# Kernel tuning notes

Hardware: AMD Instinct MI355X
Metric: run time of the kernel (lower is better)

The kernel has to match this reference:

```python
import jax, jax.numpy as jnp
import numpy as np

D_MODEL, D_STATE, HEAD_DIM, EXPAND, K, N_GROUPS = 1024, 128, 64, 2, 4, 1
D_INNER = EXPAND * D_MODEL            # 2048
N_HEADS = D_INNER // HEAD_DIM         # 32
D_PROJ = 2 * D_INNER + 2 * N_GROUPS * D_STATE + N_HEADS  # 4384
EPS = 1e-6


def setup_inputs() -> dict:
    key = jax.random.key(0)
    ks = jax.random.split(key, 8)
    B, L = 2, 2048
    x = jax.random.normal(ks[0], (B, L, D_MODEL), dtype=jnp.float32)
    norm_w = jnp.ones((D_MODEL,), jnp.float32)
    in_proj_w = jax.random.normal(ks[1], (D_PROJ, D_MODEL), jnp.float32) * (D_MODEL ** -0.5)
    conv_w = jax.random.normal(ks[2], (D_INNER, 1, K), jnp.float32) * (K ** -0.5)
    conv_b = jnp.zeros((D_INNER,), jnp.float32)
    A_log = jnp.log(jax.random.uniform(ks[3], (N_HEADS,)) * 15.0 + 1.0)
    D = jnp.ones((N_HEADS,), jnp.float32)
    dt_bias = jnp.log(jax.random.uniform(ks[4], (N_HEADS,)) * 0.099 + 0.001)
    out_proj_w = jax.random.normal(ks[5], (D_MODEL, D_INNER), jnp.float32) * (D_INNER ** -0.5)
    return {"x": x, "norm_w": norm_w, "in_proj_w": in_proj_w, "conv_w": conv_w,
            "conv_b": conv_b, "A_log": A_log, "D": D, "dt_bias": dt_bias,
            "out_proj_w": out_proj_w}


def _silu(v):
    return v * jax.nn.sigmoid(v)


def reference(x, norm_w, in_proj_w, conv_w, conv_b, A_log, D, dt_bias, out_proj_w):
    Bsz, L, _ = x.shape
    residual = x
    # RMSNorm (pre-norm)
    xn = x * jax.lax.rsqrt(jnp.mean(x * x, axis=-1, keepdims=True) + EPS) * norm_w
    proj = xn @ in_proj_w.T                                     # (B, L, D_PROJ)
    # split fused projection -> (z, x_ssm, B, C, dt_raw)
    i = 0
    z = proj[..., i:i + D_INNER]; i += D_INNER
    x_ssm = proj[..., i:i + D_INNER]; i += D_INNER
    bc = N_GROUPS * D_STATE
    Bm = proj[..., i:i + bc].reshape(Bsz, L, N_GROUPS, D_STATE); i += bc
    Cm = proj[..., i:i + bc].reshape(Bsz, L, N_GROUPS, D_STATE); i += bc
    dt_raw = proj[..., i:i + N_HEADS]
    # causal depthwise conv1d (torch pad=K-1 then slice [:L] == left-pad K-1)
    xc = jnp.transpose(x_ssm, (0, 2, 1))                        # (B, D_INNER, L)
    xc = jax.lax.conv_general_dilated(
        xc, conv_w, window_strides=(1,), padding=[(K - 1, 0)],
        dimension_numbers=("NCH", "OIH", "NCH"), feature_group_count=D_INNER)
    xc = xc + conv_b[None, :, None]
    x_conv = _silu(jnp.transpose(xc, (0, 2, 1)))                # (B, L, D_INNER)
    # discretisation
    dt = jax.nn.softplus(dt_raw + dt_bias)                      # (B, L, H)
    dA = jnp.exp(-jnp.exp(A_log)[None, None, :] * dt)           # (B, L, H)
    x_heads = x_conv.reshape(Bsz, L, N_HEADS, HEAD_DIM)
    dt_x = dt[..., None] * x_heads                              # (B, L, H, P)
    group_idx = jnp.arange(N_HEADS) // (N_HEADS // N_GROUPS)
    Bg = Bm[:, :, group_idx, :]                                 # (B, L, H, N)
    Cg = Cm[:, :, group_idx, :]
    # sequential selective scan over time via lax.scan (fp32 state)
    def step(h, inp):
        dA_t, dtx_t, B_t, C_t = inp                             # (B,H),(B,H,P),(B,H,N),(B,H,N)
        h = h * dA_t[..., None, None] + dtx_t[..., None] * B_t[:, :, None, :]
        y_t = jnp.einsum("bhpn,bhn->bhp", h, C_t)
        return h, y_t
    h0 = jnp.zeros((Bsz, N_HEADS, HEAD_DIM, D_STATE), jnp.float32)
    xs = (jnp.moveaxis(dA, 1, 0).astype(jnp.float32),
          jnp.moveaxis(dt_x, 1, 0).astype(jnp.float32),
          jnp.moveaxis(Bg, 1, 0).astype(jnp.float32),
          jnp.moveaxis(Cg, 1, 0).astype(jnp.float32))
    _, y = jax.lax.scan(step, h0, xs)                           # y: (L, B, H, P)
    y = jnp.moveaxis(y, 0, 1).astype(x.dtype)                   # (B, L, H, P)
    y = y + D[None, None, :, None] * x_heads
    y = y.reshape(Bsz, L, D_INNER) * _silu(z)                   # gated output
    return residual + y @ out_proj_w.T
```

## Files before the change

kernel.cpp:

```cpp
#include <hip/hip_runtime.h>
#include <math.h>

#define B_SZ     2
#define L_SEQ    2048
#define DM       1024
#define DP       4384
#define PS       4480
#define DI       2048
#define NH       32
#define HD       64
#define DS       128
#define M_ROWS   (B_SZ * L_SEQ)
#define QCH      64
#define NC       (L_SEQ / QCH)

typedef __bf16 bf16x8 __attribute__((ext_vector_type(8)));
typedef __bf16 bf16x4 __attribute__((ext_vector_type(4)));
typedef __bf16 bf16x2 __attribute__((ext_vector_type(2)));
typedef float  f32x4  __attribute__((ext_vector_type(4)));

__device__ __forceinline__ void gload16(const void* g, void* l) {
    __builtin_amdgcn_global_load_lds(
        (const __attribute__((address_space(1))) unsigned int*)g,
        (__attribute__((address_space(3))) unsigned int*)l,
        16, 0, 0);
}

__global__ __launch_bounds__(256) void k_prep(const float* __restrict__ Wp,
                                              __bf16* __restrict__ Wpb,
                                              const float* __restrict__ x,
                                              const float* __restrict__ w,
                                              __bf16* __restrict__ xn) {
    int tid = threadIdx.x;
    if (blockIdx.x < 4384) {
        int i = blockIdx.x * 256 + tid;
        float4 v = ((const float4*)Wp)[i];
        bf16x4 o = { (__bf16)v.x, (__bf16)v.y, (__bf16)v.z, (__bf16)v.w };
        ((bf16x4*)Wpb)[i] = o;
        return;
    }
    int row = blockIdx.x - 4384;
    const float4* x4 = (const float4*)(x + (long)row * DM);
    float4 v = x4[tid];
    float ss = v.x * v.x + v.y * v.y + v.z * v.z + v.w * v.w;
    #pragma unroll
    for (int off = 32; off > 0; off >>= 1) ss += __shfl_xor(ss, off, 64);
    __shared__ float sred[4];
    if ((tid & 63) == 0) sred[tid >> 6] = ss;
    __syncthreads();
    float tot = sred[0] + sred[1] + sred[2] + sred[3];
    float scale = rsqrtf(tot * (1.0f / (float)DM) + 1e-6f);
    const float4* w4 = (const float4*)w;
    float4 wv = w4[tid];
    bf16x4 o = { (__bf16)(v.x * scale * wv.x), (__bf16)(v.y * scale * wv.y),
                 (__bf16)(v.z * scale * wv.z), (__bf16)(v.w * scale * wv.w) };
    ((bf16x4*)(xn + (long)row * DM))[tid] = o;
}

__global__ __launch_bounds__(256) void k_gemm_bf(const __bf16* __restrict__ A,
                                                 const __bf16* __restrict__ W,
                                                 __bf16* __restrict__ Cb,
                                                 float* __restrict__ Dt,
                                                 int Nw, int K, int ldc) {
    __shared__ __align__(16) __bf16 As[2][128 * 64];
    __shared__ __align__(16) __bf16 Bs[2][128 * 64];
    int t = threadIdx.x;

    int gx = gridDim.x;
    int nwg = gx * gridDim.y;
    int orig = blockIdx.y * gx + blockIdx.x;
    int wgid = (nwg & 7) ? orig : ((orig & 7) * (nwg >> 3) + (orig >> 3));
    int bx = wgid % gx, by = wgid / gx;
    int bm = by * 128, bn = bx * 128;

    int lane = t & 63, w = t >> 6;

    int rl = lane >> 3;
    int lc = (lane & 7) ^ rl;
    int rbase = w * 32 + rl;
    const __bf16* Agp[4];
    const __bf16* Wgp[4];
    #pragma unroll
    for (int i = 0; i < 4; i++) {
        Agp[i] = A + (long)(bm + rbase + i * 8) * K + lc * 8;
        int rb = bn + rbase + i * 8; if (rb >= Nw) rb = Nw - 1;
        Wgp[i] = W + (long)rb * K + lc * 8;
    }

    int wm = (w & 1) * 64, wn = (w >> 1) * 64;
    int ln = lane & 15;
    int q  = lane >> 4;

    f32x4 acc[4][4] = {};

    int nst = K >> 6;

    #pragma unroll
    for (int i = 0; i < 4; i++) {
        gload16(Agp[i], As[0] + (w * 4 + i) * 512);
        gload16(Wgp[i], Bs[0] + (w * 4 + i) * 512);
    }

    int cur = 0;
    for (int s = 0; s < nst; ++s) {
        if (s + 1 < nst) {
            long k1 = (long)(s + 1) << 6;
            #pragma unroll
            for (int i = 0; i < 4; i++) {
                gload16(Agp[i] + k1, As[cur ^ 1] + (w * 4 + i) * 512);
                gload16(Wgp[i] + k1, Bs[cur ^ 1] + (w * 4 + i) * 512);
            }
            asm volatile("s_waitcnt vmcnt(8)" ::: "memory");
        } else {
            asm volatile("s_waitcnt vmcnt(0)" ::: "memory");
        }
        __builtin_amdgcn_sched_barrier(0);
        __builtin_amdgcn_s_barrier();
        __builtin_amdgcn_sched_barrier(0);
        __builtin_amdgcn_s_setprio(1);

        const __bf16* Asc = As[cur];
        const __bf16* Bsc = Bs[cur];
        #pragma unroll
        for (int h = 0; h < 2; h++) {
            int ch = (4 * h + q);
            int koff = ((ch ^ (ln & 7)) << 3);
            bf16x8 af[4], bfr[4];
            #pragma unroll
            for (int i = 0; i < 4; i++)
                af[i]  = *(const bf16x8*)(Asc + (wm + ln + i * 16) * 64 + koff);
            #pragma unroll
            for (int j = 0; j < 4; j++)
                bfr[j] = *(const bf16x8*)(Bsc + (wn + ln + j * 16) * 64 + koff);
            #pragma unroll
            for (int i = 0; i < 4; i++)
                #pragma unroll
                for (int j = 0; j < 4; j++)
                    acc[i][j] = __builtin_amdgcn_mfma_f32_16x16x32_bf16(
                                    af[i], bfr[j], acc[i][j], 0, 0, 0);
        }
        __builtin_amdgcn_s_setprio(0);
        __builtin_amdgcn_sched_barrier(0);
        __builtin_amdgcn_s_barrier();
        __builtin_amdgcn_sched_barrier(0);
        cur ^= 1;
    }

    int colbase = bn + wn + ln;
    #pragma unroll
    for (int i = 0; i < 4; i++) {
        #pragma unroll
        for (int r = 0; r < 4; r++) {
            int m = bm + wm + i * 16 + (lane >> 4) * 4 + r;
            long off = (long)m * ldc + colbase;
            #pragma unroll
            for (int j = 0; j < 4; j++) {
                float v = acc[i][j][r];
                Cb[off + j * 16] = (__bf16)v;
                int col = colbase + j * 16;
                if (col >= 4352 && col < 4384)
                    Dt[(long)m * 32 + (col - 4352)] = v;
            }
        }
    }
}

__global__ __launch_bounds__(256) void k_gemm_out(const __bf16* __restrict__ A,
                                                  const __bf16* __restrict__ W,
                                                  const float* __restrict__ resid,
                                                  float* __restrict__ Cf,
                                                  int K, int ldc) {
    __shared__ __align__(16) __bf16 As[2][64 * 64];
    __shared__ __align__(16) __bf16 Bs[2][128 * 64];
    int t = threadIdx.x;

    int gx = gridDim.x;
    int nwg = gx * gridDim.y;
    int orig = blockIdx.y * gx + blockIdx.x;
    int wgid = (nwg & 7) ? orig : ((orig & 7) * (nwg >> 3) + (orig >> 3));
    int bx = wgid % gx, by = wgid / gx;
    int bm = by * 64, bn = bx * 128;

    int lane = t & 63, w = t >> 6;

    int rl = lane >> 3;
    int lc = (lane & 7) ^ rl;
    const __bf16* Agp[2];
    const __bf16* Wgp[4];
    #pragma unroll
    for (int i = 0; i < 2; i++)
        Agp[i] = A + (long)(bm + w * 16 + i * 8 + rl) * K + lc * 8;
    #pragma unroll
    for (int i = 0; i < 4; i++)
        Wgp[i] = W + (long)(bn + w * 32 + i * 8 + rl) * K + lc * 8;

    int wm = (w & 1) * 32, wn = (w >> 1) * 64;
    int ln = lane & 15;
    int q  = lane >> 4;

    f32x4 acc[2][4] = {};

    int nst = K >> 6;

    #pragma unroll
    for (int i = 0; i < 2; i++) gload16(Agp[i], As[0] + (w * 2 + i) * 512);
    #pragma unroll
    for (int i = 0; i < 4; i++) gload16(Wgp[i], Bs[0] + (w * 4 + i) * 512);

    int cur = 0;
    for (int s = 0; s < nst; ++s) {
        if (s + 1 < nst) {
            long k1 = (long)(s + 1) << 6;
            #pragma unroll
            for (int i = 0; i < 2; i++)
                gload16(Agp[i] + k1, As[cur ^ 1] + (w * 2 + i) * 512);
            #pragma unroll
            for (int i = 0; i < 4; i++)
                gload16(Wgp[i] + k1, Bs[cur ^ 1] + (w * 4 + i) * 512);
            asm volatile("s_waitcnt vmcnt(6)" ::: "memory");
        } else {
            asm volatile("s_waitcnt vmcnt(0)" ::: "memory");
        }
        __builtin_amdgcn_sched_barrier(0);
        __builtin_amdgcn_s_barrier();
        __builtin_amdgcn_sched_barrier(0);
        __builtin_amdgcn_s_setprio(1);

        const __bf16* Asc = As[cur];
        const __bf16* Bsc = Bs[cur];
        #pragma unroll
        for (int h = 0; h < 2; h++) {
            int ch = (4 * h + q);
            int koff = ((ch ^ (ln & 7)) << 3);
            bf16x8 af[2], bfr[4];
            #pragma unroll
            for (int i = 0; i < 2; i++)
                af[i]  = *(const bf16x8*)(Asc + (wm + ln + i * 16) * 64 + koff);
            #pragma unroll
            for (int j = 0; j < 4; j++)
                bfr[j] = *(const bf16x8*)(Bsc + (wn + ln + j * 16) * 64 + koff);
            #pragma unroll
            for (int i = 0; i < 2; i++)
                #pragma unroll
                for (int j = 0; j < 4; j++)
                    acc[i][j] = __builtin_amdgcn_mfma_f32_16x16x32_bf16(
                                    af[i], bfr[j], acc[i][j], 0, 0, 0);
        }
        __builtin_amdgcn_s_setprio(0);
        __builtin_amdgcn_sched_barrier(0);
        __builtin_amdgcn_s_barrier();
        __builtin_amdgcn_sched_barrier(0);
        cur ^= 1;
    }

    int colbase = bn + wn + ln;
    #pragma unroll
    for (int i = 0; i < 2; i++) {
        #pragma unroll
        for (int r = 0; r < 4; r++) {
            int m = bm + wm + i * 16 + (lane >> 4) * 4 + r;
            long off = (long)m * ldc + colbase;
            #pragma unroll
            for (int j = 0; j < 4; j++) {
                float v = acc[i][j][r] + resid[off + j * 16];
                Cf[off + j * 16] = v;
            }
        }
    }
}

__global__ __launch_bounds__(256) void k_chunk(const __bf16* __restrict__ projb,
                                               const float* __restrict__ dtraw,
                                               const float* __restrict__ cw,
                                               const float* __restrict__ cb,
                                               const float* __restrict__ A_log,
                                               const float* __restrict__ dt_bias,
                                               const float* __restrict__ Dv,
                                               float* __restrict__ clog,
                                               __bf16* __restrict__ yssm,
                                               __bf16* __restrict__ Sloc) {
    int blk = blockIdx.x;
    int c  = blk & 31;
    int hh = (blk >> 5) & 31;
    int b  = blk >> 10;
    int tid = threadIdx.x;
    long rowbase = (long)b * L_SEQ + c * QCH;

    __shared__ __align__(16) __bf16 sB[64 * 136];
    __shared__ __align__(16) __bf16 sU[128 * 72];
    __shared__ __align__(16) __bf16 sXT[64 * 72];
    __shared__ __align__(16) __bf16 sXCM[67 * 72];
    __shared__ __align__(16) __bf16 sXCo[64 * 72];
    __shared__ float sCW[256];
    __shared__ float sCB[64];
    __shared__ float sclog[64];
    __shared__ float sdt[64];
    __shared__ float sw[64];

    #pragma unroll
    for (int j = 0; j < 4; j++) {
        int off = j * 256 + tid;
        int t  = off >> 4;
        int n8 = (off & 15) * 8;
        const __bf16* pr = projb + (rowbase + t) * (long)PS;
        *(bf16x8*)&sB[t * 136 + n8] = *(const bf16x8*)(pr + 4096 + n8);
        *(bf16x8*)&sU[t * 136 + n8] = *(const bf16x8*)(pr + 4224 + n8);
    }
    #pragma unroll
    for (int j = 0; j < 3; j++) {
        int off = j * 256 + tid;
        if (off < 536) {
            int ss = off >> 3;
            int p8 = (off & 7) * 8;
            bf16x8 xv;
            #pragma unroll
            for (int k = 0; k < 8; k++) xv[k] = (__bf16)0.0f;
            if (c > 0 || ss >= 3)
                xv = *(const bf16x8*)(projb + (rowbase + ss - 3) * (long)PS + DI + hh * HD + p8);
            *(bf16x8*)&sXCM[ss * 72 + p8] = xv;
        }
    }
    sCW[tid] = cw[hh * 256 + tid];
    if (tid < 64) sCB[tid] = cb[hh * 64 + tid];

    if (tid < 64) {
        float xr = dtraw[(rowbase + tid) * 32 + hh] + dt_bias[hh];
        float dt = (xr > 20.0f) ? xr : log1pf(expf(xr));
        float la = -expf(A_log[hh]);
        float v = la * dt;
        #pragma unroll
        for (int off = 1; off < 64; off <<= 1) {
            float u = __shfl_up(v, off, 64);
            if (tid >= off) v += u;
        }
        sdt[tid] = dt;
        sclog[tid] = v;
        clog[(rowbase + tid) * NH + hh] = v;
    }
    __syncthreads();

    {
        int p8 = (tid & 7) * 8;
        float wreg[8][4], breg[8];
        #pragma unroll
        for (int e = 0; e < 8; e++) {
            breg[e] = sCB[p8 + e];
            #pragma unroll
            for (int j = 0; j < 4; j++) wreg[e][j] = sCW[(p8 + e) * 4 + j];
        }
        #pragma unroll
        for (int i = 0; i < 2; i++) {
            int s = i * 32 + (tid >> 3);
            bf16x8 r0 = *(const bf16x8*)&sXCM[(s + 0) * 72 + p8];
            bf16x8 r1 = *(const bf16x8*)&sXCM[(s + 1) * 72 + p8];
            bf16x8 r2 = *(const bf16x8*)&sXCM[(s + 2) * 72 + p8];
            bf16x8 r3 = *(const bf16x8*)&sXCM[(s + 3) * 72 + p8];
            float dts = sdt[s];
            bf16x8 oc;
            #pragma unroll
            for (int e = 0; e < 8; e++) {
                float acc = breg[e];
                acc = fmaf(wreg[e][0], (float)r0[e], acc);
                acc = fmaf(wreg[e][1], (float)r1[e], acc);
                acc = fmaf(wreg[e][2], (float)r2[e], acc);
                acc = fmaf(wreg[e][3], (float)r3[e], acc);
                float xc = acc / (1.0f + expf(-acc));
                oc[e] = (__bf16)xc;
                sXT[(p8 + e) * 72 + s] = (__bf16)(dts * xc);
            }
            *(bf16x8*)&sXCo[s * 72 + p8] = oc;
        }
    }
    if (tid < 64) sw[tid] = expf(sclog[63] - sclog[tid]);
    __syncthreads();

    int lane = tid & 63, w = tid >> 6;
    int ln = lane & 15;
    int quad = lane >> 4;
    int kc = quad * 8;

    bf16x8 caf[4];
    #pragma unroll
    for (int k0 = 0; k0 < 4; k0++)
        caf[k0] = *(const bf16x8*)&sU[(16 * w + ln) * 136 + kc + k0 * 32];
    f32x4 g[4] = {};
    #pragma unroll
    for (int j = 0; j < 4; j++)
        #pragma unroll
        for (int k0 = 0; k0 < 4; k0++) {
            bf16x8 bf_ = *(const bf16x8*)&sB[(16 * j + ln) * 136 + kc + k0 * 32];
            g[j] = __builtin_amdgcn_mfma_f32_16x16x32_bf16(caf[k0], bf_, g[j], 0, 0, 0);
        }

    {
        int trow = 16 * w + quad * 4;
        #pragma unroll
        for (int r = 0; r < 4; r++) {
            int t = trow + r;
            float ct = sclog[t];
            #pragma unroll
            for (int j = 0; j < 4; j++) {
                int s = 16 * j + ln;
                float v = (s <= t) ? g[j][r] * expf(ct - sclog[s]) : 0.0f;
                sXCM[t * 72 + s] = (__bf16)v;
            }
        }
    }
    __syncthreads();

    #pragma unroll
    for (int j = 0; j < 4; j++) {
        int s  = tid & 63;
        int n8 = (j * 4 + (tid >> 6)) * 8;
        bf16x8 v = *(const bf16x8*)&sB[s * 136 + n8];
        #pragma unroll
        for (int k = 0; k < 8; k++) sU[(n8 + k) * 72 + s] = v[k];
    }

    {
        float Dh = Dv[hh];
        bf16x8 maf[2];
        #pragma unroll
        for (int k0 = 0; k0 < 2; k0++)
            maf[k0] = *(const bf16x8*)&sXCM[(16 * w + ln) * 72 + kc + k0 * 32];
        f32x4 y[4] = {};
        #pragma unroll
        for (int j = 0; j < 4; j++)
            #pragma unroll
            for (int k0 = 0; k0 < 2; k0++) {
                bf16x8 xf = *(const bf16x8*)&sXT[(16 * j + ln) * 72 + kc + k0 * 32];
                y[j] = __builtin_amdgcn_mfma_f32_16x16x32_bf16(maf[k0], xf, y[j], 0, 0, 0);
            }
        #pragma unroll
        for (int j = 0; j < 4; j++)
            #pragma unroll
            for (int r = 0; r < 4; r++) {
                int t = 16 * w + quad * 4 + r;
                int p = 16 * j + ln;
                float v = y[j][r] + Dh * (float)sXCo[t * 72 + p];
                yssm[(rowbase + t) * DI + hh * HD + p] = (__bf16)v;
            }
    }
    __syncthreads();

    {
        bf16x8 xaf[2];
        #pragma unroll
        for (int k0 = 0; k0 < 2; k0++) {
            bf16x8 raw = *(const bf16x8*)&sXT[(16 * w + ln) * 72 + kc + k0 * 32];
            bf16x8 sc;
            #pragma unroll
            for (int jj = 0; jj < 8; jj++) {
                int s = kc + k0 * 32 + jj;
                sc[jj] = (__bf16)((float)raw[jj] * sw[s]);
            }
            xaf[k0] = sc;
        }
        f32x4 sacc[8] = {};
        #pragma unroll
        for (int j = 0; j < 8; j++)
            #pragma unroll
            for (int k0 = 0; k0 < 2; k0++) {
                bf16x8 btf = *(const bf16x8*)&sU[(16 * j + ln) * 72 + kc + k0 * 32];
                sacc[j] = __builtin_amdgcn_mfma_f32_16x16x32_bf16(xaf[k0], btf, sacc[j], 0, 0, 0);
            }
        long sbase = ((long)(b * NH + hh) * NC + c) * (HD * DS);
        #pragma unroll
        for (int j = 0; j < 8; j++)
            #pragma unroll
            for (int r = 0; r < 4; r++) {
                int p = 16 * w + quad * 4 + r;
                int n = 16 * j + ln;
                Sloc[sbase + p * DS + n] = (__bf16)sacc[j][r];
            }
    }
}

__global__ __launch_bounds__(256) void k_carry_f2b(__bf16* __restrict__ Sloc,
                                                   const float* __restrict__ clog,
                                                   const float* __restrict__ Wo,
                                                   __bf16* __restrict__ Wob) {
    int bid = blockIdx.x;
    int tid = threadIdx.x;
    if (bid >= 1024) {
        int i = (bid - 1024) * 256 + tid;
        float4 v = ((const float4*)Wo)[i];
        bf16x4 o = { (__bf16)v.x, (__bf16)v.y, (__bf16)v.z, (__bf16)v.w };
        ((bf16x4*)Wob)[i] = o;
        return;
    }
    int idx = bid * 256 + tid;
    int n2 = idx & 63;
    int p  = (idx >> 6) & 63;
    int hh = (idx >> 12) & 31;
    int b  = idx >> 17;

    __shared__ float slam[NC];
    if (tid < NC)
        slam[tid] = expf(clog[((long)b * L_SEQ + tid * QCH + QCH - 1) * NH + hh]);
    __syncthreads();

    long base = ((long)(b * NH + hh) * NC) * (HD * DS) + p * DS + n2 * 2;
    const long cstride = HD * DS;
    float T0 = 0.0f, T1 = 0.0f;
    long a = base;
    bf16x2 Sv = *(const bf16x2*)&Sloc[a];
    for (int c = 0; c < NC; c++) {
        bf16x2 Sn;
        if (c + 1 < NC) Sn = *(const bf16x2*)&Sloc[a + cstride];
        float lam = slam[c];
        bf16x2 Tv = { (__bf16)T0, (__bf16)T1 };
        *(bf16x2*)&Sloc[a] = Tv;
        T0 = fmaf(T0, lam, (float)Sv[0]);
        T1 = fmaf(T1, lam, (float)Sv[1]);
        Sv = Sn;
        a += cstride;
    }
}

__global__ __launch_bounds__(256, 4) void k_fix(const __bf16* __restrict__ projb,
                                                const __bf16* __restrict__ Sloc,
                                                const float* __restrict__ clog,
                                                const __bf16* __restrict__ yb,
                                                __bf16* __restrict__ yg) {
    int blk = blockIdx.x;
    int c  = blk & 31;
    int hh = (blk >> 5) & 31;
    int b  = blk >> 10;

    __shared__ __align__(16) __bf16 sC[64 * 136];
    __shared__ __align__(16) __bf16 sH[64 * 136];
    __shared__ float sP[64];

    int tid = threadIdx.x;
    long hbase = ((long)(b * NH + hh) * NC + c) * (HD * DS);
    long rowbase = (long)b * L_SEQ + c * QCH;

    #pragma unroll
    for (int j = 0; j < 4; j++) {
        int off = j * 256 + tid;
        int t  = off >> 4;
        int n8 = (off & 15) * 8;
        *(bf16x8*)&sC[t * 136 + n8] =
            *(const bf16x8*)(projb + (rowbase + t) * (long)PS + 4224 + n8);
    }
    #pragma unroll
    for (int j = 0; j < 4; j++) {
        int off = j * 256 + tid;
        int p  = off >> 4;
        int n8 = (off & 15) * 8;
        *(bf16x8*)&sH[p * 136 + n8] = *(const bf16x8*)&Sloc[hbase + (long)off * 8];
    }
    if (tid < 64) sP[tid] = expf(clog[(rowbase + tid) * NH + hh]);
    __syncthreads();

    int lane = tid & 63, w = tid >> 6;
    int ln = lane & 15;
    int quad = lane >> 4;
    int kc = quad * 8;

    bf16x8 caf[4];
    #pragma unroll
    for (int k0 = 0; k0 < 4; k0++)
        caf[k0] = *(const bf16x8*)&sC[(16 * w + ln) * 136 + kc + k0 * 32];
    f32x4 acc4[4] = {};
    #pragma unroll
    for (int j = 0; j < 4; j++)
        #pragma unroll
        for (int k0 = 0; k0 < 4; k0++) {
            bf16x8 hf = *(const bf16x8*)&sH[(16 * j + ln) * 136 + kc + k0 * 32];
            acc4[j] = __builtin_amdgcn_mfma_f32_16x16x32_bf16(caf[k0], hf, acc4[j], 0, 0, 0);
        }

    #pragma unroll
    for (int j = 0; j < 4; j++)
        #pragma unroll
        for (int r = 0; r < 4; r++) {
            int t = 16 * w + quad * 4 + r;
            int p = 16 * j + ln;
            long row = rowbase + t;
            long yoff = row * DI + hh * HD + p;
            float pm = sP[t];
            float z = (float)projb[row * (long)PS + hh * HD + p];
            float o = ((float)yb[yoff] + pm * acc4[j][r]) * (z / (1.0f + expf(-z)));
            yg[yoff] = (__bf16)o;
        }
}

extern "C" void kernel_launch(void* const* d_in, const int* in_sizes, int n_in,
                              void* d_out, int out_size, void* d_ws, size_t ws_size,
                              hipStream_t stream) {
    const float* x       = (const float*)d_in[0];
    const float* norm_w  = (const float*)d_in[1];
    const float* Wp      = (const float*)d_in[2];
    const float* cw      = (const float*)d_in[3];
    const float* cb      = (const float*)d_in[4];
    const float* A_log   = (const float*)d_in[5];
    const float* Dv      = (const float*)d_in[6];
    const float* dt_bias = (const float*)d_in[7];
    const float* Wo      = (const float*)d_in[8];
    float* out = (float*)d_out;

    float* ws     = (float*)d_ws;
    __bf16* projb = (__bf16*)ws;
    float* dtraw  = ws    + 9175040;
    float* clog   = dtraw + 131072;
    float* ybh    = clog  + 131072;
    float* ybf    = ybh   + 4194304;
    float* wob_s  = ybf   + 4194304;
    float* U      = wob_s + 1048576;

    __bf16* xnb  = (__bf16*)U;
    __bf16* Wpb  = (__bf16*)(U + 2097152);
    __bf16* Sloc = (__bf16*)U;
    __bf16* Wob  = (__bf16*)wob_s;
    __bf16* ybb  = (__bf16*)ybf;
    __bf16* yb   = (__bf16*)ybh;

    k_prep<<<4384 + M_ROWS, 256, 0, stream>>>(Wp, Wpb, x, norm_w, xnb);
    {
        dim3 g(PS / 128, M_ROWS / 128);
        k_gemm_bf<<<g, 256, 0, stream>>>(xnb, Wpb, projb, dtraw, DP, DM, PS);
    }

    k_chunk<<<B_SZ * NH * NC, 256, 0, stream>>>(projb, dtraw, cw, cb, A_log,
                                                dt_bias, Dv, clog, yb, Sloc);
    k_carry_f2b<<<3072, 256, 0, stream>>>(Sloc, clog, Wo, Wob);
    k_fix<<<B_SZ * NH * NC, 256, 0, stream>>>(projb, Sloc, clog, yb, ybb);

    {
        dim3 g(DM / 128, M_ROWS / 64);
        k_gemm_out<<<g, 256, 0, stream>>>(ybb, Wob, x, out, DI, DM);
    }
}
```

Baseline: 262.2 us.

## Remap GEMM workgroups per XCD and async-load B/C chunk tiles with XOR swizzle

Both GEMM kernels get a hardcoded workgroup-to-tile mapping for their specific grid shapes. Tiles are grouped so that workgroups sharing an XCD cover a compact block of rows and columns, with the aim of better L2 reuse. The chunk kernel now loads its B and C tiles with direct global-to-LDS loads into an unpadded 128-wide layout, using an XOR swizzle to avoid bank conflicts. All readers of those tiles are updated to match the swizzle. This removes the register round-trip and the padding, but the fast path only applies to specific grid dimensions.

Result: faster. 257.1 us (-2.0%).

```diff
diff --git a/kernel.cpp b/kernel.cpp
--- a/kernel.cpp
+++ b/kernel.cpp
@@ -69,8 +69,18 @@
     int gx = gridDim.x;
     int nwg = gx * gridDim.y;
     int orig = blockIdx.y * gx + blockIdx.x;
-    int wgid = (nwg & 7) ? orig : ((orig & 7) * (nwg >> 3) + (orig >> 3));
-    int bx = wgid % gx, by = wgid / gx;
+    int bx, by;
+    if (gx == 35 && gridDim.y == 32) {
+        int sy = orig & 7;
+        int k  = orig >> 3;
+        int st = k / 20;
+        int wv = k % 20;
+        bx = st * 5 + wv % 5;
+        by = sy * 4 + wv / 5;
+    } else {
+        int wgid = (nwg & 7) ? orig : ((orig & 7) * (nwg >> 3) + (orig >> 3));
+        bx = wgid % gx; by = wgid / gx;
+    }
     int bm = by * 128, bn = bx * 128;
 
     int lane = t & 63, w = t >> 6;
@@ -177,8 +187,18 @@
     int gx = gridDim.x;
     int nwg = gx * gridDim.y;
     int orig = blockIdx.y * gx + blockIdx.x;
-    int wgid = (nwg & 7) ? orig : ((orig & 7) * (nwg >> 3) + (orig >> 3));
-    int bx = wgid % gx, by = wgid / gx;
+    int bx, by;
+    if (gx == 8 && gridDim.y == 64) {
+        int xcd = orig & 7;
+        int k   = orig >> 3;
+        int st  = k >> 3;
+        int wv  = k & 7;
+        bx = (st & 3) * 2 + (wv & 1);
+        by = xcd * 8 + (st >> 2) * 4 + (wv >> 1);
+    } else {
+        int wgid = (nwg & 7) ? orig : ((orig & 7) * (nwg >> 3) + (orig >> 3));
+        bx = wgid % gx; by = wgid / gx;
+    }
     int bm = by * 64, bn = bx * 128;
 
     int lane = t & 63, w = t >> 6;
@@ -286,7 +306,7 @@
     int tid = threadIdx.x;
     long rowbase = (long)b * L_SEQ + c * QCH;
 
-    __shared__ __align__(16) __bf16 sB[64 * 136];
+    __shared__ __align__(16) __bf16 sB[64 * 128];
     __shared__ __align__(16) __bf16 sU[128 * 72];
     __shared__ __align__(16) __bf16 sXT[64 * 72];
     __shared__ __align__(16) __bf16 sXCM[67 * 72];
@@ -297,14 +317,20 @@
     __shared__ float sdt[64];
     __shared__ float sw[64];
 
-    #pragma unroll
-    for (int j = 0; j < 4; j++) {
-        int off = j * 256 + tid;
-        int t  = off >> 4;
-        int n8 = (off & 15) * 8;
-        const __bf16* pr = projb + (rowbase + t) * (long)PS;
-        *(bf16x8*)&sB[t * 136 + n8] = *(const bf16x8*)(pr + 4096 + n8);
-        *(bf16x8*)&sU[t * 136 + n8] = *(const bf16x8*)(pr + 4224 + n8);
+    int lane = tid & 63, w = tid >> 6;
+
+    {
+        int rl4 = lane >> 4;
+        int pc  = lane & 15;
+        #pragma unroll
+        for (int r = 0; r < 4; r++) {
+            int row0 = r * 16 + w * 4;
+            int row  = row0 + rl4;
+            int lc2  = (pc ^ (row & 7)) * 8;
+            const __bf16* pr = projb + (rowbase + row) * (long)PS;
+            gload16(pr + 4096 + lc2, sB + row0 * 128);
+            gload16(pr + 4224 + lc2, sU + row0 * 128);
+        }
     }
     #pragma unroll
     for (int j = 0; j < 3; j++) {
@@ -374,7 +400,6 @@
     if (tid < 64) sw[tid] = expf(sclog[63] - sclog[tid]);
     __syncthreads();
 
-    int lane = tid & 63, w = tid >> 6;
     int ln = lane & 15;
     int quad = lane >> 4;
     int kc = quad * 8;
@@ -382,13 +407,13 @@
     bf16x8 caf[4];
     #pragma unroll
     for (int k0 = 0; k0 < 4; k0++)
-        caf[k0] = *(const bf16x8*)&sU[(16 * w + ln) * 136 + kc + k0 * 32];
+        caf[k0] = *(const bf16x8*)&sU[(16 * w + ln) * 128 + (((quad + 4 * k0) ^ (ln & 7)) << 3)];
     f32x4 g[4] = {};
     #pragma unroll
     for (int j = 0; j < 4; j++)
         #pragma unroll
         for (int k0 = 0; k0 < 4; k0++) {
-            bf16x8 bf_ = *(const bf16x8*)&sB[(16 * j + ln) * 136 + kc + k0 * 32];
+            bf16x8 bf_ = *(const bf16x8*)&sB[(16 * j + ln) * 128 + (((quad + 4 * k0) ^ (ln & 7)) << 3)];
             g[j] = __builtin_amdgcn_mfma_f32_16x16x32_bf16(caf[k0], bf_, g[j], 0, 0, 0);
         }
 
@@ -411,8 +436,9 @@
     #pragma unroll
     for (int j = 0; j < 4; j++) {
         int s  = tid & 63;
-        int n8 = (j * 4 + (tid >> 6)) * 8;
-        bf16x8 v = *(const bf16x8*)&sB[s * 136 + n8];
+        int ch = j * 4 + (tid >> 6);
+        bf16x8 v = *(const bf16x8*)&sB[s * 128 + ((ch ^ (s & 7)) << 3)];
+        int n8 = ch * 8;
         #pragma unroll
         for (int k = 0; k < 8; k++) sU[(n8 + k) * 72 + s] = v[k];
     }
```
